# Kernel optimization log

Hardware: AMD Instinct MI355X
Metric: run time of the kernel (lower is better)

Reference implementation:

```python
import jax, jax.numpy as jnp
import numpy as np

NEAR = 0.2          # near-plane cull, matches uvd[...,2] >= 0.2 in the source
SIGMA2_MAX = 9.0    # 3-sigma disk extent, matches get_disks' sigma3 corners
ALPHA_MIN = 1.0 / 255.0


def quat_to_rot(q):
    """Unit-quaternion [P,4] (w,x,y,z) -> rotation matrices [P,3,3]."""
    q = q / (jnp.linalg.norm(q, axis=-1, keepdims=True) + 1e-12)
    w, x, y, z = q[..., 0], q[..., 1], q[..., 2], q[..., 3]
    r0 = jnp.stack([1 - 2 * (y * y + z * z), 2 * (x * y - w * z), 2 * (x * z + w * y)], -1)
    r1 = jnp.stack([2 * (x * y + w * z), 1 - 2 * (x * x + z * z), 2 * (y * z - w * x)], -1)
    r2 = jnp.stack([2 * (x * z - w * y), 2 * (y * z + w * x), 1 - 2 * (x * x + y * y)], -1)
    return jnp.stack([r0, r1, r2], -2)


def setup_inputs() -> dict:
    key = jax.random.key(0)
    k = jax.random.split(key, 6)
    H = W = 128
    P = 4096
    tanfov = 0.4
    f = W / (2.0 * tanfov)
    xs = (jnp.arange(W, dtype=jnp.float32) - (W - 1) / 2.0) / f
    ys = (jnp.arange(H, dtype=jnp.float32) - (H - 1) / 2.0) / f
    gx, gy = jnp.meshgrid(xs, ys, indexing='xy')
    d = jnp.stack([gx, gy, jnp.ones_like(gx)], -1)
    ray_d = d / jnp.linalg.norm(d, axis=-1, keepdims=True)   # [H,W,3]
    ray_o = jnp.zeros((H, W, 3), jnp.float32)
    means3D = jax.random.normal(k[0], (P, 3), jnp.float32) * 1.5 + jnp.array([0.0, 0.0, 4.0], jnp.float32)
    scales = jax.random.uniform(k[1], (P, 2), jnp.float32, 0.02, 0.15)
    rotations = jax.random.normal(k[2], (P, 4), jnp.float32)
    opacities = jax.random.uniform(k[3], (P, 1), jnp.float32, 0.3, 1.0)
    colors = jax.random.uniform(k[4], (P, 3), jnp.float32)
    bg_color = jnp.zeros((3,), jnp.float32)
    return dict(ray_o=ray_o, ray_d=ray_d, means3D=means3D, scales=scales,
                rotations=rotations, opacities=opacities, colors=colors, bg_color=bg_color)


def reference(ray_o, ray_d, means3D, scales, rotations, opacities, colors, bg_color):
    """Gaussian-surfel ray tracing: ray/disk-plane intersection, 2D Gaussian
    falloff in the surfel tangent frame, front-to-back alpha compositing in
    depth order (the math the BVH-accelerated SurfelTracer computes)."""
    H, W, _ = ray_o.shape
    ro = ray_o.reshape(-1, 3)
    rd = ray_d.reshape(-1, 3)
    R = quat_to_rot(rotations)                     # [P,3,3]
    tu, tv, nrm = R[..., :, 0], R[..., :, 1], R[..., :, 2]  # tangent frame columns

    # ray-plane intersection t = dot(mu - o, n) / dot(d, n)  -> [Nr,P]
    den = rd @ nrm.T
    num = jnp.einsum('pk,pk->p', means3D, nrm)[None, :] - ro @ nrm.T
    safe_den = jnp.where(jnp.abs(den) < 1e-8, 1e-8, den)
    t = num / safe_den

    # local disk coords u,v of hit point without materializing [Nr,P,3]
    u = (ro @ tu.T - jnp.einsum('pk,pk->p', means3D, tu)[None, :] + t * (rd @ tu.T)) / scales[None, :, 0]
    v = (ro @ tv.T - jnp.einsum('pk,pk->p', means3D, tv)[None, :] + t * (rd @ tv.T)) / scales[None, :, 1]
    r2 = u * u + v * v
    G = jnp.exp(-0.5 * r2)
    alpha = jnp.clip(opacities[None, :, 0] * G, 0.0, 0.99)
    valid = (t > NEAR) & (r2 < SIGMA2_MAX) & (jnp.abs(den) > 1e-8) & (alpha > ALPHA_MIN)
    alpha = jnp.where(valid, alpha, 0.0)

    # front-to-back compositing: sort hits by depth per ray
    t_key = jnp.where(valid, t, jnp.inf)
    order = jnp.argsort(t_key, axis=1)
    alpha_s = jnp.take_along_axis(alpha, order, axis=1)
    trans = jnp.cumprod(1.0 - alpha_s, axis=1)
    trans = jnp.concatenate([jnp.ones_like(trans[:, :1]), trans[:, :-1]], axis=1)  # exclusive
    w_s = alpha_s * trans
    inv = jnp.argsort(order, axis=1)
    w = jnp.take_along_axis(w_s, inv, axis=1)      # weights in original surfel order

    acc = w.sum(-1)                                # [Nr]
    rgb = w @ colors + (1.0 - acc)[:, None] * bg_color[None, :]
    dpt = (w * jnp.where(valid, t, 0.0)).sum(-1)
    norm = w @ nrm
    return (rgb.reshape(H, W, 3), dpt.reshape(H, W, 1),
            acc.reshape(H, W, 1), norm.reshape(H, W, 3))
```

## Files before the change

kernel.cpp:

```cpp
#include <hip/hip_runtime.h>
#include <stdint.h>

#define NEAR_T  0.2f
#define SIG2MAX 9.0f
#define AMIN    (1.0f/255.0f)
#define NSL     16
#define TILE    16
#define KFIX    64


__device__ __forceinline__ float dot3(float ax,float ay,float az,
                                      float bx,float by,float bz){
  return fmaf(ax,bx, fmaf(ay,by, az*bz));
}

__device__ __forceinline__ bool eval_hit(const float* __restrict__ gp,
    float rox,float roy,float roz, float rdx,float rdy,float rdz,
    float& t_out, float& a_out)
{
  float nx=gp[6], ny=gp[7], nz=gp[8];
  float den  = dot3(rdx,rdy,rdz, nx,ny,nz);
  float aden = fabsf(den);
  float num  = gp[11] - dot3(rox,roy,roz, nx,ny,nz);
  float sden = (aden < 1e-8f) ? 1e-8f : den;
  float t = __fdividef(num, sden);
  float ru = dot3(rox,roy,roz, gp[0],gp[1],gp[2]);
  float du = dot3(rdx,rdy,rdz, gp[0],gp[1],gp[2]);
  float u  = fmaf(t, du, ru - gp[9])  * gp[12];
  float rv = dot3(rox,roy,roz, gp[3],gp[4],gp[5]);
  float dv = dot3(rdx,rdy,rdz, gp[3],gp[4],gp[5]);
  float v  = fmaf(t, dv, rv - gp[10]) * gp[13];
  float r2 = fmaf(u,u, v*v);
  float G  = __expf(-0.5f*r2);
  float a  = fminf(gp[14]*G, 0.99f);
  t_out = t; a_out = a;
  return (t > NEAR_T) & (r2 < SIG2MAX) & (aden > 1e-8f) & (a > AMIN);
}

__device__ __forceinline__ unsigned long long make_key(float t, float a, uint32_t g){
  uint32_t a16 = (uint32_t)(a * 65535.f + 0.5f);
  return ((unsigned long long)__float_as_uint(t) << 32) |
         ((unsigned long long)a16 << 16) | (unsigned long long)g;
}

__global__ void k_prep(const float* __restrict__ rot, const float* __restrict__ means,
                       const float* __restrict__ scales, const float* __restrict__ opac,
                       const float* __restrict__ colors, const float* __restrict__ ray_o,
                       const float* __restrict__ ray_d,
                       float* __restrict__ geo, float* __restrict__ col,
                       float* __restrict__ baux, uint32_t* __restrict__ misc,
                       int P, int npix, int W)
{
  int tid = blockIdx.x*blockDim.x + threadIdx.x;
  float g0x = ray_d[0]/ray_d[2], g0y = ray_d[1]/ray_d[2];
  float axm = ray_d[3]/ray_d[5] - g0x;
  float aym = ray_d[(size_t)W*3+1]/ray_d[(size_t)W*3+2] - g0y;
  if (tid == 0){
    float* mf = (float*)misc;
    mf[1] = axm; mf[2] = g0x; mf[3] = aym; mf[4] = g0y;
    if (!(fabsf(axm) > 1e-12f) || !(fabsf(aym) > 1e-12f)) atomicOr(misc, 1u);
  }
  if (tid < npix){
    int ix = tid % W, iy = tid / W;
    float rox=ray_o[tid*3+0], roy=ray_o[tid*3+1], roz=ray_o[tid*3+2];
    float rdx=ray_d[tid*3+0], rdy=ray_d[tid*3+1], rdz=ray_d[tid*3+2];
    bool ok = (rox==0.f) & (roy==0.f) & (roz==0.f) & (rdz > 0.8f);
    if (ok){
      float gx = rdx/rdz, gy = rdy/rdz;
      ok = (fabsf(gx - fmaf(axm,(float)ix,g0x)) <= 3e-4f) &
           (fabsf(gy - fmaf(aym,(float)iy,g0y)) <= 3e-4f);
    }
    if (!ok) atomicOr(misc, 1u);
  }
  if (tid < P){
    float qw=rot[tid*4+0], qx=rot[tid*4+1], qy=rot[tid*4+2], qz=rot[tid*4+3];
    float n = sqrtf(qw*qw+qx*qx+qy*qy+qz*qz) + 1e-12f;
    qw/=n; qx/=n; qy/=n; qz/=n;
    float tux = 1.f-2.f*(qy*qy+qz*qz), tuy = 2.f*(qx*qy+qw*qz), tuz = 2.f*(qx*qz-qw*qy);
    float tvx = 2.f*(qx*qy-qw*qz), tvy = 1.f-2.f*(qx*qx+qz*qz), tvz = 2.f*(qy*qz+qw*qx);
    float nx  = 2.f*(qx*qz+qw*qy), ny  = 2.f*(qy*qz-qw*qx), nz  = 1.f-2.f*(qx*qx+qy*qy);
    float mx=means[tid*3+0], my=means[tid*3+1], mz=means[tid*3+2];
    float sx=scales[tid*2+0], sy=scales[tid*2+1];
    float* gp = &geo[(size_t)tid*16];
    gp[0]=tux; gp[1]=tuy; gp[2]=tuz;
    gp[3]=tvx; gp[4]=tvy; gp[5]=tvz;
    gp[6]=nx;  gp[7]=ny;  gp[8]=nz;
    gp[9]  = mx*tux+my*tuy+mz*tuz;
    gp[10] = mx*tvx+my*tvy+mz*tvz;
    gp[11] = mx*nx +my*ny +mz*nz;
    gp[12] = 1.f/sx;
    gp[13] = 1.f/sy;
    gp[14] = opac[tid];
    gp[15] = 0.f;
    col[tid*3+0]=colors[tid*3+0]; col[tid*3+1]=colors[tid*3+1]; col[tid*3+2]=colors[tid*3+2];
    float* bp = &baux[(size_t)tid*8];
    const float R3 = 3.02f;
    bp[0]=mx; bp[1]=my; bp[2]=mz;
    bp[3]=R3*(sx*fabsf(tux)+sy*fabsf(tvx));
    bp[4]=R3*(sx*fabsf(tuy)+sy*fabsf(tvy));
    bp[5]=R3*(sx*fabsf(tuz)+sy*fabsf(tvz));
    bp[6]=0.f; bp[7]=0.f;
  }
}

__device__ __forceinline__ bool tile_range(const float* __restrict__ bp,
    bool fallback, float axm, float bxm, float aym, float bym,
    int W, int H, int TX, int TY,
    int& tx0, int& tx1, int& ty0, int& ty1)
{
  if (fallback){ tx0=0; tx1=TX-1; ty0=0; ty1=TY-1; return true; }
  float mx=bp[0], my=bp[1], mz=bp[2], ex=bp[3], ey=bp[4], ez=bp[5];
  float zmin=mz-ez, zmax=mz+ez;
  if (zmax <= 0.16f) return false;
  if (zmin <= 1e-3f){ tx0=0; tx1=TX-1; ty0=0; ty1=TY-1; return true; }
  float xmin=mx-ex, xmax=mx+ex, ymin=my-ey, ymax=my+ey;
  float gxmin = (xmin>=0.f)? xmin/zmax : xmin/zmin;
  float gxmax = (xmax>=0.f)? xmax/zmin : xmax/zmax;
  float gymin = (ymin>=0.f)? ymin/zmax : ymin/zmin;
  float gymax = (ymax>=0.f)? ymax/zmin : ymax/zmax;
  float p0 = (gxmin - bxm)/axm, p1 = (gxmax - bxm)/axm;
  float q0 = (gymin - bym)/aym, q1 = (gymax - bym)/aym;
  int ix0 = (int)floorf(fminf(p0,p1)) - 1;
  int ix1 = (int)ceilf (fmaxf(p0,p1)) + 1;
  int iy0 = (int)floorf(fminf(q0,q1)) - 1;
  int iy1 = (int)ceilf (fmaxf(q0,q1)) + 1;
  if (ix1 < 0 || ix0 > W-1 || iy1 < 0 || iy0 > H-1) return false;
  tx0 = max(ix0,0)/TILE; tx1 = min(ix1,W-1)/TILE;
  ty0 = max(iy0,0)/TILE; ty1 = min(iy1,H-1)/TILE;
  return true;
}

__global__ __launch_bounds__(1024)
void k_bin_fused(const float* __restrict__ baux, const uint32_t* __restrict__ misc,
                 uint32_t* __restrict__ tileOff, uint32_t* __restrict__ tileList,
                 int P, int W, int H, int TX, int TY)
{
  __shared__ uint32_t sCnt[1024];
  __shared__ uint32_t sOff[1025];
  int NT = TX*TY;
  int tid = threadIdx.x;
  for (int i=tid; i<NT; i+=1024) sCnt[i]=0u;
  __syncthreads();
  const float* mf = (const float*)misc;
  bool fb = (misc[0] != 0u);
  float a1=mf[1], a2=mf[2], a3=mf[3], a4=mf[4];
  for (int g=tid; g<P; g+=1024){
    int tx0,tx1,ty0,ty1;
    if (tile_range(&baux[(size_t)g*8], fb, a1,a2,a3,a4, W,H,TX,TY, tx0,tx1,ty0,ty1)){
      for (int ty=ty0; ty<=ty1; ++ty)
        for (int tx=tx0; tx<=tx1; ++tx)
          atomicAdd(&sCnt[ty*TX+tx], 1u);
    }
  }
  __syncthreads();
  if (tid == 0){
    uint32_t run = 0;
    for (int i=0; i<NT; ++i){ sOff[i] = run; run += sCnt[i]; }
    sOff[NT] = run;
  }
  __syncthreads();
  for (int i=tid; i<=NT; i+=1024) tileOff[i] = sOff[i];
  for (int i=tid; i<NT;  i+=1024) sCnt[i] = sOff[i];
  __syncthreads();
  for (int g=tid; g<P; g+=1024){
    int tx0,tx1,ty0,ty1;
    if (tile_range(&baux[(size_t)g*8], fb, a1,a2,a3,a4, W,H,TX,TY, tx0,tx1,ty0,ty1)){
      for (int ty=ty0; ty<=ty1; ++ty)
        for (int tx=tx0; tx<=tx1; ++tx){
          uint32_t slot = atomicAdd(&sCnt[ty*TX+tx], 1u);
          tileList[slot] = (uint32_t)g;
        }
    }
  }
}

__global__ void k_bin_count(const float* __restrict__ baux, const uint32_t* __restrict__ misc,
                            uint32_t* __restrict__ tileCnt, int P, int W, int H, int TX, int TY)
{
  int g = blockIdx.x*blockDim.x + threadIdx.x;
  if (g >= P) return;
  const float* mf = (const float*)misc;
  bool fb = (misc[0] != 0u);
  int tx0,tx1,ty0,ty1;
  if (tile_range(&baux[(size_t)g*8], fb, mf[1],mf[2],mf[3],mf[4], W,H,TX,TY, tx0,tx1,ty0,ty1)){
    for (int ty=ty0; ty<=ty1; ++ty)
      for (int tx=tx0; tx<=tx1; ++tx)
        atomicAdd(&tileCnt[ty*TX+tx], 1u);
  }
}

__global__ __launch_bounds__(64)
void k_scan(const uint32_t* __restrict__ tileCnt, uint32_t* __restrict__ tileOff,
            uint32_t* __restrict__ tileCur, int NT)
{
  int lane = threadIdx.x;
  uint32_t run = 0;
  for (int c0=0; c0<NT; c0+=64){
    int i = c0 + lane;
    uint32_t v = (i<NT) ? tileCnt[i] : 0u;
    uint32_t inc = v;
    #pragma unroll
    for (int d=1; d<64; d<<=1){
      uint32_t o = (uint32_t)__shfl_up((int)inc, d);
      if (lane >= d) inc += o;
    }
    uint32_t excl = run + inc - v;
    if (i < NT){ tileOff[i] = excl; tileCur[i] = excl; }
    run += (uint32_t)__shfl((int)inc, 63);
  }
  if (lane == 0) tileOff[NT] = run;
}

__global__ void k_bin_fill(const float* __restrict__ baux, const uint32_t* __restrict__ misc,
                           uint32_t* __restrict__ tileCur, uint32_t* __restrict__ tileList,
                           int P, int W, int H, int TX, int TY)
{
  int g = blockIdx.x*blockDim.x + threadIdx.x;
  if (g >= P) return;
  const float* mf = (const float*)misc;
  bool fb = (misc[0] != 0u);
  int tx0,tx1,ty0,ty1;
  if (tile_range(&baux[(size_t)g*8], fb, mf[1],mf[2],mf[3],mf[4], W,H,TX,TY, tx0,tx1,ty0,ty1)){
    for (int ty=ty0; ty<=ty1; ++ty)
      for (int tx=tx0; tx<=tx1; ++tx){
        uint32_t slot = atomicAdd(&tileCur[ty*TX+tx], 1u);
        tileList[slot] = (uint32_t)g;
      }
  }
}

__global__ __launch_bounds__(256)
void k_trace(const float* __restrict__ geo, const float* __restrict__ ray_o,
             const float* __restrict__ ray_d, const uint32_t* __restrict__ tileOff,
             const uint32_t* __restrict__ tileList, uint32_t* __restrict__ cnt,
             unsigned long long* __restrict__ keys64, int W, int H, int TX)
{
  int tile = blockIdx.x;
  int tx = tile % TX, ty = tile / TX;
  int tid = threadIdx.x;
  int ix = tx*TILE + (tid & (TILE-1));
  int iy = ty*TILE + (tid / TILE);
  bool live = (ix < W) & (iy < H);
  int px = live ? (iy*W + ix) : 0;
  uint32_t base = tileOff[tile], len = tileOff[tile+1] - base;
  float rox=ray_o[px*3+0], roy=ray_o[px*3+1], roz=ray_o[px*3+2];
  float rdx=ray_d[px*3+0], rdy=ray_d[px*3+1], rdz=ray_d[px*3+2];
  for (uint32_t s = blockIdx.y; s < len; s += NSL){
    int gu = __builtin_amdgcn_readfirstlane((int)tileList[base+s]);
    const float* gp = &geo[(size_t)gu*16];
    float t,a;
    bool hit = eval_hit(gp, rox,roy,roz, rdx,rdy,rdz, t, a) && live;
    if (hit){
      uint32_t slot = atomicAdd(&cnt[px], 1u);
      if (slot < KFIX) keys64[(size_t)px*KFIX + slot] = make_key(t, a, (uint32_t)gu);
    }
  }
}

__global__ __launch_bounds__(256)
void k_classify(const uint32_t* __restrict__ cnt, uint32_t* __restrict__ bk,
                uint32_t* __restrict__ listA, uint32_t* __restrict__ listB,
                uint32_t* __restrict__ listC, int npix)
{
  int px = blockIdx.x*blockDim.x + threadIdx.x;
  int lane = threadIdx.x & 63;
  bool live = px < npix;
  uint32_t K = live ? cnt[px] : 0u;
  bool inA = live && (K <= (uint32_t)KFIX);
  bool inB = live && (K > (uint32_t)KFIX) && (K <= 512u);
  bool inC = live && (K > 512u);
  unsigned long long mA = __ballot(inA), mB = __ballot(inB), mC = __ballot(inC);
  uint32_t bA=0, bB=0, bC=0;
  if (lane == 0){
    if (mA) bA = atomicAdd(&bk[0], (uint32_t)__popcll(mA));
    if (mB) bB = atomicAdd(&bk[1], (uint32_t)__popcll(mB));
    if (mC) bC = atomicAdd(&bk[2], (uint32_t)__popcll(mC));
  }
  bA = (uint32_t)__shfl((int)bA, 0);
  bB = (uint32_t)__shfl((int)bB, 0);
  bC = (uint32_t)__shfl((int)bC, 0);
  unsigned long long lt = (1ull << lane) - 1ull;
  if (inA) listA[bA + (uint32_t)__popcll(mA & lt)] = (uint32_t)px;
  if (inB) listB[bB + (uint32_t)__popcll(mB & lt)] = (uint32_t)px;
  if (inC) listC[bC + (uint32_t)__popcll(mC & lt)] = (uint32_t)px;
}

__device__ __forceinline__ float wred(float v){
  #pragma unroll
  for (int d=32; d>0; d>>=1) v += __shfl_down(v, d);
  return v;
}

__device__ __forceinline__ void comp_write(int px, int npix, int lane,
    float r_, float g_, float bl_, float dpt_, float acc_,
    float nx_, float ny_, float nz_, const float* __restrict__ bg,
    float* __restrict__ out)
{
  r_ = wred(r_); g_ = wred(g_); bl_ = wred(bl_);
  dpt_ = wred(dpt_); acc_ = wred(acc_);
  nx_ = wred(nx_); ny_ = wred(ny_); nz_ = wred(nz_);
  if (lane == 0){
    float one_m = 1.f - acc_;
    out[(size_t)px*3+0] = r_  + one_m*bg[0];
    out[(size_t)px*3+1] = g_  + one_m*bg[1];
    out[(size_t)px*3+2] = bl_ + one_m*bg[2];
    out[(size_t)npix*3 + px] = dpt_;
    out[(size_t)npix*4 + px] = acc_;
    out[(size_t)npix*5 + (size_t)px*3+0] = nx_;
    out[(size_t)npix*5 + (size_t)px*3+1] = ny_;
    out[(size_t)npix*5 + (size_t)px*3+2] = nz_;
  }
}

__global__ __launch_bounds__(256)
void k_comp_small(const unsigned long long* __restrict__ keys64,
                  const uint32_t* __restrict__ cnt,
                  const float* __restrict__ geo, const float* __restrict__ col,
                  const float* __restrict__ bg, const uint32_t* __restrict__ listA,
                  const uint32_t* __restrict__ bk, float* __restrict__ out, int npix)
{
  int lane = threadIdx.x & 63;
  int wave = threadIdx.x >> 6;
  uint32_t n = bk[0];
  for (uint32_t li = blockIdx.x*4u + wave; li < n; li += gridDim.x*4u){
    int px = (int)listA[li];
    uint32_t K = cnt[px];
    unsigned long long key = (lane < (int)K) ? keys64[(size_t)px*KFIX + lane] : ~0ull;
    #pragma unroll
    for (int k=2; k<=64; k<<=1){
      #pragma unroll
      for (int j=k>>1; j>0; j>>=1){
        unsigned long long other = __shfl_xor(key, j);
        bool keep_min = (((lane & j) == 0) == ((lane & k) == 0));
        unsigned long long lo = key < other ? key : other;
        unsigned long long hi = key < other ? other : key;
        key = keep_min ? lo : hi;
      }
    }
    bool valid = lane < (int)K;
    const float inv65535 = 1.f/65535.f;
    float a = (float)((uint32_t)(key >> 16) & 0xFFFFu) * inv65535;
    float p = valid ? (1.f - a) : 1.f;
    float ip = p;
    #pragma unroll
    for (int d=1; d<64; d<<=1){ float v = __shfl_up(ip, d); if (lane >= d) ip *= v; }
    float T = __shfl_up(ip, 1);
    if (lane == 0) T = 1.f;
    float r_=0.f, g_=0.f, bl_=0.f, dpt_=0.f, acc_=0.f, nx_=0.f, ny_=0.f, nz_=0.f;
    if (valid){
      float t = __uint_as_float((uint32_t)(key >> 32));
      uint32_t g = (uint32_t)(key & 0xFFFFu);
      float w = a * T;
      const float* gp = &geo[(size_t)g*16];
      const float* cp = &col[(size_t)g*3];
      r_ = w*cp[0]; g_ = w*cp[1]; bl_ = w*cp[2];
      dpt_ = w*t; acc_ = w;
      nx_ = w*gp[6]; ny_ = w*gp[7]; nz_ = w*gp[8];
    }
    comp_write(px, npix, lane, r_,g_,bl_,dpt_,acc_,nx_,ny_,nz_, bg, out);
  }
}

template<int MAXK>
__global__ __launch_bounds__(64)
void k_comp_lds(const float* __restrict__ geo, const float* __restrict__ col,
                const float* __restrict__ ray_o, const float* __restrict__ ray_d,
                const uint32_t* __restrict__ tileOff, const uint32_t* __restrict__ tileList,
                const float* __restrict__ bg, const uint32_t* __restrict__ list,
                const uint32_t* __restrict__ nptr, float* __restrict__ out,
                int npix, int W, int TX)
{
  __shared__ unsigned long long sk[MAXK];
  int lane = threadIdx.x;
  unsigned long long lt = (1ull << lane) - 1ull;
  uint32_t n = nptr[0];
  for (uint32_t li = blockIdx.x; li < n; li += gridDim.x){
    int px = (int)list[li];
    int ix = px % W, iy = px / W;
    int tile = (iy/TILE)*TX + (ix/TILE);
    uint32_t base = tileOff[tile], len = tileOff[tile+1] - base;
    float rox=ray_o[px*3+0], roy=ray_o[px*3+1], roz=ray_o[px*3+2];
    float rdx=ray_d[px*3+0], rdy=ray_d[px*3+1], rdz=ray_d[px*3+2];

    uint32_t run = 0;
    for (uint32_t s0=0; s0<len; s0+=64){
      uint32_t s = s0 + (uint32_t)lane;
      bool act = s < len;
      uint32_t gu = act ? tileList[base+s] : 0u;
      float t=0.f, a=0.f;
      bool hit = false;
      if (act) hit = eval_hit(&geo[(size_t)gu*16], rox,roy,roz, rdx,rdy,rdz, t, a);
      unsigned long long m = __ballot(hit);
      if (hit){
        uint32_t slot = run + (uint32_t)__popcll(m & lt);
        if (slot < (uint32_t)MAXK) sk[slot] = make_key(t, a, gu);
      }
      run += (uint32_t)__popcll(m);
    }
    uint32_t K = min(run, (uint32_t)MAXK);
    uint32_t N = 1; while (N < K) N <<= 1;
    for (uint32_t i=K+lane; i<N; i+=64) sk[i] = ~0ull;
    __syncthreads();

    for (uint32_t kk=2; kk<=N; kk<<=1){
      for (uint32_t j=kk>>1; j>0; j>>=1){
        for (uint32_t i=lane; i<N; i+=64){
          uint32_t ij = i ^ j;
          if (ij > i){
            unsigned long long a = sk[i], b = sk[ij];
            bool up = ((i & kk) == 0);
            if ((a > b) == up){ sk[i] = b; sk[ij] = a; }
          }
        }
        __syncthreads();
      }
    }

    const float inv65535 = 1.f/65535.f;
    uint32_t C = (K + 63) >> 6;
    uint32_t b0 = lane*C, e0 = min(b0 + C, K);
    float p = 1.f;
    for (uint32_t i=b0; i<e0; ++i){
      float a = (float)((uint32_t)(sk[i] >> 16) & 0xFFFFu) * inv65535;
      p *= (1.f - a);
    }
    float ip = p;
    #pragma unroll
    for (int d=1; d<64; d<<=1){ float v = __shfl_up(ip, d); if (lane >= d) ip *= v; }
    float T = __shfl_up(ip, 1);
    if (lane == 0) T = 1.f;

    float r_=0.f, g_=0.f, bl_=0.f, dpt_=0.f, acc_=0.f, nx_=0.f, ny_=0.f, nz_=0.f;
    for (uint32_t i=b0; i<e0; ++i){
      unsigned long long key = sk[i];
      float t = __uint_as_float((uint32_t)(key >> 32));
      float a = (float)((uint32_t)(key >> 16) & 0xFFFFu) * inv65535;
      uint32_t g = (uint32_t)(key & 0xFFFFu);
      float w = a * T;
      const float* gp = &geo[(size_t)g*16];
      const float* cp = &col[(size_t)g*3];
      r_  += w * cp[0]; g_ += w * cp[1]; bl_ += w * cp[2];
      dpt_ += w * t; acc_ += w;
      nx_ += w * gp[6]; ny_ += w * gp[7]; nz_ += w * gp[8];
      T *= (1.f - a);
    }
    comp_write(px, npix, lane, r_,g_,bl_,dpt_,acc_,nx_,ny_,nz_, bg, out);
    __syncthreads();
  }
}

extern "C" void kernel_launch(void* const* d_in, const int* in_sizes, int n_in,
                              void* d_out, int out_size, void* d_ws, size_t ws_size,
                              hipStream_t stream)
{
  const float* ray_o  = (const float*)d_in[0];
  const float* ray_d  = (const float*)d_in[1];
  const float* means  = (const float*)d_in[2];
  const float* scales = (const float*)d_in[3];
  const float* rot    = (const float*)d_in[4];
  const float* opac   = (const float*)d_in[5];
  const float* colors = (const float*)d_in[6];
  const float* bg     = (const float*)d_in[7];
  float* out = (float*)d_out;

  int npix = in_sizes[0] / 3;
  int P    = in_sizes[2] / 3;
  int W    = (int)(sqrtf((float)npix) + 0.5f);
  int H    = npix / W;
  int TX   = (W + TILE - 1) / TILE;
  int TY   = (H + TILE - 1) / TILE;
  int NT   = TX * TY;

  uint8_t* ws = (uint8_t*)d_ws;
  size_t o_geo   = 0;
  size_t sz_geo  = ((size_t)P*16*4 + 255) & ~(size_t)255;
  size_t o_col   = o_geo + sz_geo;
  size_t sz_col  = ((size_t)P*3*4 + 255) & ~(size_t)255;
  size_t o_baux  = o_col + sz_col;
  size_t sz_baux = ((size_t)P*8*4 + 255) & ~(size_t)255;

  size_t o_ctrl  = o_baux + sz_baux;
  size_t sz_pix  = ((size_t)npix*4 + 255) & ~(size_t)255;
  size_t o_cnt   = o_ctrl;
  size_t sz_nt   = ((size_t)NT*4 + 255) & ~(size_t)255;
  size_t o_tcnt  = o_cnt + sz_pix;
  size_t o_misc  = o_tcnt + sz_nt;
  size_t o_bk    = o_misc + 256;
  size_t ctrl_sz = (o_bk + 256) - o_ctrl;

  size_t o_la    = o_ctrl + ctrl_sz;
  size_t o_lb    = o_la + sz_pix;
  size_t o_lc    = o_lb + sz_pix;
  size_t o_toff  = o_lc + sz_pix;
  size_t sz_toff = ((size_t)(NT+1)*4 + 255) & ~(size_t)255;
  size_t o_tcur  = o_toff + sz_toff;
  size_t o_tlist = o_tcur + sz_nt;
  size_t sz_tlist= (((size_t)P*NT*4) + 255) & ~(size_t)255;
  size_t o_k64   = o_tlist + sz_tlist;

  float*    geo     = (float*)(ws + o_geo);
  float*    col     = (float*)(ws + o_col);
  float*    baux    = (float*)(ws + o_baux);
  uint32_t* cnt     = (uint32_t*)(ws + o_cnt);
  uint32_t* tileCnt = (uint32_t*)(ws + o_tcnt);
  uint32_t* misc    = (uint32_t*)(ws + o_misc);
  uint32_t* bk      = (uint32_t*)(ws + o_bk);
  uint32_t* listA   = (uint32_t*)(ws + o_la);
  uint32_t* listB   = (uint32_t*)(ws + o_lb);
  uint32_t* listC   = (uint32_t*)(ws + o_lc);
  uint32_t* tileOff = (uint32_t*)(ws + o_toff);
  uint32_t* tileCur = (uint32_t*)(ws + o_tcur);
  uint32_t* tileList= (uint32_t*)(ws + o_tlist);
  unsigned long long* keys64 = (unsigned long long*)(ws + o_k64);

  hipMemsetAsync(ws + o_ctrl, 0, ctrl_sz, stream);

  int initN = npix > P ? npix : P;
  k_prep<<<(initN + 255)/256, 256, 0, stream>>>(rot, means, scales, opac, colors,
                                                ray_o, ray_d, geo, col, baux, misc,
                                                P, npix, W);
  if (NT <= 1024){
    k_bin_fused<<<1, 1024, 0, stream>>>(baux, misc, tileOff, tileList, P, W, H, TX, TY);
  } else {
    k_bin_count<<<(P + 255)/256, 256, 0, stream>>>(baux, misc, tileCnt, P, W, H, TX, TY);
    k_scan<<<1, 64, 0, stream>>>(tileCnt, tileOff, tileCur, NT);
    k_bin_fill<<<(P + 255)/256, 256, 0, stream>>>(baux, misc, tileCur, tileList,
                                                  P, W, H, TX, TY);
  }
  dim3 tgrid(NT, NSL);
  k_trace<<<tgrid, 256, 0, stream>>>(geo, ray_o, ray_d, tileOff, tileList, cnt,
                                     keys64, W, H, TX);
  k_classify<<<(npix + 255)/256, 256, 0, stream>>>(cnt, bk, listA, listB, listC, npix);
  k_comp_small<<<1024, 256, 0, stream>>>(keys64, cnt, geo, col, bg, listA, bk, out, npix);
  k_comp_lds<512><<<2048, 64, 0, stream>>>(geo, col, ray_o, ray_d, tileOff, tileList,
                                           bg, listB, bk+1, out, npix, W, TX);
  k_comp_lds<4096><<<256, 64, 0, stream>>>(geo, col, ray_o, ray_d, tileOff, tileList,
                                           bg, listC, bk+2, out, npix, W, TX);
}
```

Baseline: 143.0 us.

## Shrink trace tiles to 8x8 and drop pixel classification in favour of in-kernel filtering

Trace tiles shrink from 16x16 to 8x8 pixels, so each block is a single 64-lane wave, and the slice count drops to 8. The smaller tiles mean fewer surfels per tile and less wasted intersection work. The classify kernel and its pixel lists are removed. Both compositing kernels now scan every pixel and skip those outside their count range. The two LDS compositing variants are merged into one 4096-entry kernel, so medium-count pixels now run with the larger shared buffer and possibly lower occupancy. Grid-stride scans that skip most pixels add some wasted work in exchange for two fewer launches.

After: 187.3 us. 31.0% more time.

```diff
diff --git a/kernel.cpp b/kernel.cpp
--- a/kernel.cpp
+++ b/kernel.cpp
@@ -4,8 +4,8 @@
 #define NEAR_T  0.2f
 #define SIG2MAX 9.0f
 #define AMIN    (1.0f/255.0f)
-#define NSL     16
-#define TILE    16
+#define NSL     8
+#define TILE    8
 #define KFIX    64
 
 
@@ -229,7 +229,7 @@
   }
 }
 
-__global__ __launch_bounds__(256)
+__global__ __launch_bounds__(64)
 void k_trace(const float* __restrict__ geo, const float* __restrict__ ray_o,
              const float* __restrict__ ray_d, const uint32_t* __restrict__ tileOff,
              const uint32_t* __restrict__ tileList, uint32_t* __restrict__ cnt,
@@ -237,9 +237,9 @@
 {
   int tile = blockIdx.x;
   int tx = tile % TX, ty = tile / TX;
-  int tid = threadIdx.x;
-  int ix = tx*TILE + (tid & (TILE-1));
-  int iy = ty*TILE + (tid / TILE);
+  int lane = threadIdx.x;
+  int ix = tx*TILE + (lane & (TILE-1));
+  int iy = ty*TILE + (lane / TILE);
   bool live = (ix < W) & (iy < H);
   int px = live ? (iy*W + ix) : 0;
   uint32_t base = tileOff[tile], len = tileOff[tile+1] - base;
@@ -257,34 +257,6 @@
   }
 }
 
-__global__ __launch_bounds__(256)
-void k_classify(const uint32_t* __restrict__ cnt, uint32_t* __restrict__ bk,
-                uint32_t* __restrict__ listA, uint32_t* __restrict__ listB,
-                uint32_t* __restrict__ listC, int npix)
-{
-  int px = blockIdx.x*blockDim.x + threadIdx.x;
-  int lane = threadIdx.x & 63;
-  bool live = px < npix;
-  uint32_t K = live ? cnt[px] : 0u;
-  bool inA = live && (K <= (uint32_t)KFIX);
-  bool inB = live && (K > (uint32_t)KFIX) && (K <= 512u);
-  bool inC = live && (K > 512u);
-  unsigned long long mA = __ballot(inA), mB = __ballot(inB), mC = __ballot(inC);
-  uint32_t bA=0, bB=0, bC=0;
-  if (lane == 0){
-    if (mA) bA = atomicAdd(&bk[0], (uint32_t)__popcll(mA));
-    if (mB) bB = atomicAdd(&bk[1], (uint32_t)__popcll(mB));
-    if (mC) bC = atomicAdd(&bk[2], (uint32_t)__popcll(mC));
-  }
-  bA = (uint32_t)__shfl((int)bA, 0);
-  bB = (uint32_t)__shfl((int)bB, 0);
-  bC = (uint32_t)__shfl((int)bC, 0);
-  unsigned long long lt = (1ull << lane) - 1ull;
-  if (inA) listA[bA + (uint32_t)__popcll(mA & lt)] = (uint32_t)px;
-  if (inB) listB[bB + (uint32_t)__popcll(mB & lt)] = (uint32_t)px;
-  if (inC) listC[bC + (uint32_t)__popcll(mC & lt)] = (uint32_t)px;
-}
-
 __device__ __forceinline__ float wred(float v){
   #pragma unroll
   for (int d=32; d>0; d>>=1) v += __shfl_down(v, d);
@@ -316,15 +288,13 @@
 void k_comp_small(const unsigned long long* __restrict__ keys64,
                   const uint32_t* __restrict__ cnt,
                   const float* __restrict__ geo, const float* __restrict__ col,
-                  const float* __restrict__ bg, const uint32_t* __restrict__ listA,
-                  const uint32_t* __restrict__ bk, float* __restrict__ out, int npix)
+                  const float* __restrict__ bg, float* __restrict__ out, int npix)
 {
   int lane = threadIdx.x & 63;
   int wave = threadIdx.x >> 6;
-  uint32_t n = bk[0];
-  for (uint32_t li = blockIdx.x*4u + wave; li < n; li += gridDim.x*4u){
-    int px = (int)listA[li];
+  for (int px = (int)(blockIdx.x*4u + wave); px < npix; px += (int)(gridDim.x*4u)){
     uint32_t K = cnt[px];
+    if (K > (uint32_t)KFIX) continue;
     unsigned long long key = (lane < (int)K) ? keys64[(size_t)px*KFIX + lane] : ~0ull;
     #pragma unroll
     for (int k=2; k<=64; k<<=1){
@@ -361,21 +331,18 @@
   }
 }
 
-template<int MAXK>
 __global__ __launch_bounds__(64)
-void k_comp_lds(const float* __restrict__ geo, const float* __restrict__ col,
-                const float* __restrict__ ray_o, const float* __restrict__ ray_d,
-                const uint32_t* __restrict__ tileOff, const uint32_t* __restrict__ tileList,
-                const float* __restrict__ bg, const uint32_t* __restrict__ list,
-                const uint32_t* __restrict__ nptr, float* __restrict__ out,
-                int npix, int W, int TX)
-{
-  __shared__ unsigned long long sk[MAXK];
+void k_comp_over(const float* __restrict__ geo, const float* __restrict__ col,
+                 const float* __restrict__ ray_o, const float* __restrict__ ray_d,
+                 const uint32_t* __restrict__ tileOff, const uint32_t* __restrict__ tileList,
+                 const uint32_t* __restrict__ cnt, const float* __restrict__ bg,
+                 float* __restrict__ out, int npix, int W, int TX)
+{
+  __shared__ unsigned long long sk[4096];
   int lane = threadIdx.x;
   unsigned long long lt = (1ull << lane) - 1ull;
-  uint32_t n = nptr[0];
-  for (uint32_t li = blockIdx.x; li < n; li += gridDim.x){
-    int px = (int)list[li];
+  for (int px = (int)blockIdx.x; px < npix; px += (int)gridDim.x){
+    if (cnt[px] <= (uint32_t)KFIX) continue;
     int ix = px % W, iy = px / W;
     int tile = (iy/TILE)*TX + (ix/TILE);
     uint32_t base = tileOff[tile], len = tileOff[tile+1] - base;
@@ -393,11 +360,11 @@
       unsigned long long m = __ballot(hit);
       if (hit){
         uint32_t slot = run + (uint32_t)__popcll(m & lt);
-        if (slot < (uint32_t)MAXK) sk[slot] = make_key(t, a, gu);
+        if (slot < 4096u) sk[slot] = make_key(t, a, gu);
       }
       run += (uint32_t)__popcll(m);
     }
-    uint32_t K = min(run, (uint32_t)MAXK);
+    uint32_t K = min(run, 4096u);
     uint32_t N = 1; while (N < K) N <<= 1;
     for (uint32_t i=K+lane; i<N; i+=64) sk[i] = ~0ull;
     __syncthreads();
@@ -485,13 +452,9 @@
   size_t sz_nt   = ((size_t)NT*4 + 255) & ~(size_t)255;
   size_t o_tcnt  = o_cnt + sz_pix;
   size_t o_misc  = o_tcnt + sz_nt;
-  size_t o_bk    = o_misc + 256;
-  size_t ctrl_sz = (o_bk + 256) - o_ctrl;
-
-  size_t o_la    = o_ctrl + ctrl_sz;
-  size_t o_lb    = o_la + sz_pix;
-  size_t o_lc    = o_lb + sz_pix;
-  size_t o_toff  = o_lc + sz_pix;
+  size_t ctrl_sz = (o_misc + 256) - o_ctrl;
+
+  size_t o_toff  = o_ctrl + ctrl_sz;
   size_t sz_toff = ((size_t)(NT+1)*4 + 255) & ~(size_t)255;
   size_t o_tcur  = o_toff + sz_toff;
   size_t o_tlist = o_tcur + sz_nt;
@@ -504,10 +467,6 @@
   uint32_t* cnt     = (uint32_t*)(ws + o_cnt);
   uint32_t* tileCnt = (uint32_t*)(ws + o_tcnt);
   uint32_t* misc    = (uint32_t*)(ws + o_misc);
-  uint32_t* bk      = (uint32_t*)(ws + o_bk);
-  uint32_t* listA   = (uint32_t*)(ws + o_la);
-  uint32_t* listB   = (uint32_t*)(ws + o_lb);
-  uint32_t* listC   = (uint32_t*)(ws + o_lc);
   uint32_t* tileOff = (uint32_t*)(ws + o_toff);
   uint32_t* tileCur = (uint32_t*)(ws + o_tcur);
   uint32_t* tileList= (uint32_t*)(ws + o_tlist);
@@ -528,12 +487,9 @@
                                                   P, W, H, TX, TY);
   }
   dim3 tgrid(NT, NSL);
-  k_trace<<<tgrid, 256, 0, stream>>>(geo, ray_o, ray_d, tileOff, tileList, cnt,
-                                     keys64, W, H, TX);
-  k_classify<<<(npix + 255)/256, 256, 0, stream>>>(cnt, bk, listA, listB, listC, npix);
-  k_comp_small<<<1024, 256, 0, stream>>>(keys64, cnt, geo, col, bg, listA, bk, out, npix);
-  k_comp_lds<512><<<2048, 64, 0, stream>>>(geo, col, ray_o, ray_d, tileOff, tileList,
-                                           bg, listB, bk+1, out, npix, W, TX);
-  k_comp_lds<4096><<<256, 64, 0, stream>>>(geo, col, ray_o, ray_d, tileOff, tileList,
-                                           bg, listC, bk+2, out, npix, W, TX);
-}
+  k_trace<<<tgrid, 64, 0, stream>>>(geo, ray_o, ray_d, tileOff, tileList, cnt,
+                                    keys64, W, H, TX);
+  k_comp_small<<<1024, 256, 0, stream>>>(keys64, cnt, geo, col, bg, out, npix);
+  k_comp_over<<<1024, 64, 0, stream>>>(geo, col, ray_o, ray_d, tileOff, tileList,
+                                       cnt, bg, out, npix, W, TX);
+}
```
